# Kernel tuning notes

Hardware: AMD Instinct MI355X
Metric: run time of the kernel (lower is better)

Reference implementation:

```python
import jax, jax.numpy as jnp
import numpy as np


def setup_inputs() -> dict:
    key = jax.random.key(0)
    VOCAB = 50257
    BATCH, SEQ = 512, 8192
    assignments = jax.random.randint(key, (BATCH, SEQ), 0, VOCAB, dtype=jnp.int64 if jax.config.jax_enable_x64 else jnp.int32)
    return {"assignments": assignments, "vocab_size": VOCAB}


def reference(assignments, vocab_size):
    # Faithful math: counts[b, v] = sum_t (assignments[b, t] == v), then
    # frequency = counts / counts.sum(-1, keepdim=True).
    # Implemented as a per-row scatter-add histogram (same result, no O(N*V*S) blowup).
    def _hist(row):  # row: [seq] int -> [vocab] float32
        return jnp.zeros((vocab_size,), dtype=jnp.float32).at[row].add(1.0)

    counts = jax.vmap(_hist)(assignments)  # [batch, vocab]
    frequency = counts / counts.sum(axis=-1, keepdims=True)
    return frequency
```

## Files before the change

kernel.cpp:

```cpp
#include <hip/hip_runtime.h>


#define TF_BLOCK 256
#define TF_CHUNK 12800
#define TF_NCHUNK 4
#define TF_VPT 32

__global__ __launch_bounds__(TF_BLOCK)
void XTermFrequency_hist_kernel(const int* __restrict__ assign,
                                float* __restrict__ out,
                                int V, int S, float scale) {
    __shared__ unsigned int hist[TF_CHUNK];
    const int row = blockIdx.x;
    const int tid = threadIdx.x;

    const int4* rowp = (const int4*)(assign + (long long)row * S);
    int4 vals[TF_VPT / 4];
#pragma unroll
    for (int k = 0; k < TF_VPT / 4; ++k) {
        vals[k] = rowp[tid + k * TF_BLOCK];
    }

    float* __restrict__ orow = out + (long long)row * V;

    for (int c = 0; c < TF_NCHUNK; ++c) {
        const int base = c * TF_CHUNK;
        const int len = min(V - base, TF_CHUNK);

        for (int i = tid; i < TF_CHUNK; i += TF_BLOCK) hist[i] = 0u;
        __syncthreads();

#pragma unroll
        for (int k = 0; k < TF_VPT / 4; ++k) {
            const int4 v4 = vals[k];
            unsigned int d;
            d = (unsigned int)(v4.x - base);
            if (d < (unsigned int)TF_CHUNK) atomicAdd(&hist[d], 1u);
            d = (unsigned int)(v4.y - base);
            if (d < (unsigned int)TF_CHUNK) atomicAdd(&hist[d], 1u);
            d = (unsigned int)(v4.z - base);
            if (d < (unsigned int)TF_CHUNK) atomicAdd(&hist[d], 1u);
            d = (unsigned int)(v4.w - base);
            if (d < (unsigned int)TF_CHUNK) atomicAdd(&hist[d], 1u);
        }
        __syncthreads();

        for (int i = tid; i < len; i += TF_BLOCK) {
            orow[base + i] = (float)hist[i] * scale;
        }
        __syncthreads();
    }
}

extern "C" void kernel_launch(void* const* d_in, const int* in_sizes, int n_in,
                              void* d_out, int out_size, void* d_ws, size_t ws_size,
                              hipStream_t stream) {
    const int* assign = (const int*)d_in[0];
    float* out = (float*)d_out;

    const int V = 50257;
    const int B = out_size / V;
    const int S = in_sizes[0] / B;
    const float scale = 1.0f / (float)S;

    XTermFrequency_hist_kernel<<<dim3(B), dim3(TF_BLOCK), 0, stream>>>(
        assign, out, V, S, scale);
}
```

Before: 117.8 us.

## Split vocab chunks across a 2D grid and vectorize histogram output stores

The vocab dimension moves out of the serial in-block loop and onto a second grid dimension. There are 8 chunks of 6400 bins, so there are eight times as many blocks, each with a smaller shared histogram. Output writes become aligned float4 stores, with scalar head and tail handling. In exchange, each block re-reads the full input row, so input traffic grows eightfold unless L2 absorbs the reuse.

```diff
diff --git a/kernel.cpp b/kernel.cpp
--- a/kernel.cpp
+++ b/kernel.cpp
@@ -2,9 +2,9 @@
 
 
 #define TF_BLOCK 256
-#define TF_CHUNK 12800
-#define TF_NCHUNK 4
-#define TF_VPT 32
+#define TF_CHUNK 6400
+#define TF_NCHUNK 8
+#define TF_I4PT 8
 
 __global__ __launch_bounds__(TF_BLOCK)
 void XTermFrequency_hist_kernel(const int* __restrict__ assign,
@@ -12,44 +12,53 @@
                                 int V, int S, float scale) {
     __shared__ unsigned int hist[TF_CHUNK];
     const int row = blockIdx.x;
+    const int base = blockIdx.y * TF_CHUNK;
+    const int len = min(V - base, TF_CHUNK);
     const int tid = threadIdx.x;
 
-    const int4* rowp = (const int4*)(assign + (long long)row * S);
-    int4 vals[TF_VPT / 4];
+    for (int i = tid; i < TF_CHUNK; i += TF_BLOCK) hist[i] = 0u;
+
+    const int4* rowp = (const int4*)(assign + (size_t)row * S);
+    int4 v[TF_I4PT];
 #pragma unroll
-    for (int k = 0; k < TF_VPT / 4; ++k) {
-        vals[k] = rowp[tid + k * TF_BLOCK];
+    for (int k = 0; k < TF_I4PT; ++k) v[k] = rowp[tid + k * TF_BLOCK];
+
+    __syncthreads();
+
+#pragma unroll
+    for (int k = 0; k < TF_I4PT; ++k) {
+        unsigned int d;
+        d = (unsigned int)(v[k].x - base);
+        if (d < (unsigned int)TF_CHUNK) atomicAdd(&hist[d], 1u);
+        d = (unsigned int)(v[k].y - base);
+        if (d < (unsigned int)TF_CHUNK) atomicAdd(&hist[d], 1u);
+        d = (unsigned int)(v[k].z - base);
+        if (d < (unsigned int)TF_CHUNK) atomicAdd(&hist[d], 1u);
+        d = (unsigned int)(v[k].w - base);
+        if (d < (unsigned int)TF_CHUNK) atomicAdd(&hist[d], 1u);
+    }
+    __syncthreads();
+
+    float* dst = out + (size_t)row * V + base;
+    int head = (int)((4u - (((unsigned int)(size_t)dst >> 2) & 3u)) & 3u);
+    if (head > len) head = len;
+    if (tid < head) dst[tid] = (float)hist[tid] * scale;
+
+    const int n4 = (len - head) >> 2;
+    float4* __restrict__ dst4 = (float4*)(dst + head);
+    for (int j = tid; j < n4; j += TF_BLOCK) {
+        const int i = head + 4 * j;
+        float4 o;
+        o.x = (float)hist[i]     * scale;
+        o.y = (float)hist[i + 1] * scale;
+        o.z = (float)hist[i + 2] * scale;
+        o.w = (float)hist[i + 3] * scale;
+        dst4[j] = o;
     }
 
-    float* __restrict__ orow = out + (long long)row * V;
-
-    for (int c = 0; c < TF_NCHUNK; ++c) {
-        const int base = c * TF_CHUNK;
-        const int len = min(V - base, TF_CHUNK);
-
-        for (int i = tid; i < TF_CHUNK; i += TF_BLOCK) hist[i] = 0u;
-        __syncthreads();
-
-#pragma unroll
-        for (int k = 0; k < TF_VPT / 4; ++k) {
-            const int4 v4 = vals[k];
-            unsigned int d;
-            d = (unsigned int)(v4.x - base);
-            if (d < (unsigned int)TF_CHUNK) atomicAdd(&hist[d], 1u);
-            d = (unsigned int)(v4.y - base);
-            if (d < (unsigned int)TF_CHUNK) atomicAdd(&hist[d], 1u);
-            d = (unsigned int)(v4.z - base);
-            if (d < (unsigned int)TF_CHUNK) atomicAdd(&hist[d], 1u);
-            d = (unsigned int)(v4.w - base);
-            if (d < (unsigned int)TF_CHUNK) atomicAdd(&hist[d], 1u);
-        }
-        __syncthreads();
-
-        for (int i = tid; i < len; i += TF_BLOCK) {
-            orow[base + i] = (float)hist[i] * scale;
-        }
-        __syncthreads();
-    }
+    const int done = head + 4 * n4;
+    const int rem = len - done;
+    if (tid < rem) dst[done + tid] = (float)hist[done + tid] * scale;
 }
 
 extern "C" void kernel_launch(void* const* d_in, const int* in_sizes, int n_in,
@@ -63,6 +72,6 @@
     const int S = in_sizes[0] / B;
     const float scale = 1.0f / (float)S;
 
-    XTermFrequency_hist_kernel<<<dim3(B), dim3(TF_BLOCK), 0, stream>>>(
+    XTermFrequency_hist_kernel<<<dim3(B, TF_NCHUNK), dim3(TF_BLOCK), 0, stream>>>(
         assign, out, V, S, scale);
 }
```

New measurement: 120.9 us. +2.6%, slower.
